# Kernel tuning notes

Hardware: AMD Instinct MI355X
Metric: run time of the kernel (lower is better)

Reference implementation:

```python
import jax, jax.numpy as jnp
import numpy as np

SPLINE_ORDER = 3


def _bspline_basis(x, knots, k, order):
    """Cox-de Boor recursion with static (python float) knots, matching the torch code exactly."""
    if order == 0:
        if k + 1 >= len(knots):
            return jnp.zeros_like(x)
        return ((knots[k] <= x) & (x < knots[k + 1])).astype(x.dtype)
    left = 0.0
    right = 0.0
    if k + order < len(knots) and knots[k + order] != knots[k]:
        left = (x - knots[k]) / (knots[k + order] - knots[k]) * _bspline_basis(x, knots, k, order - 1)
    if k + order + 1 < len(knots) and knots[k + order + 1] != knots[k + 1]:
        right = (knots[k + order + 1] - x) / (knots[k + order + 1] - knots[k + 1]) * _bspline_basis(x, knots, k + 1, order - 1)
    return left + right


def setup_inputs() -> dict:
    key = jax.random.key(0)
    k1, k2, k3 = jax.random.split(key, 3)
    B, S, IN, OUT, NUM_KNOTS = 16, 4096, 256, 256, 5
    x = jax.random.normal(k1, (B, S, IN), dtype=jnp.float32)
    inner_coeffs = jax.random.normal(k2, (IN, NUM_KNOTS), dtype=jnp.float32) * 0.1
    outer_coeffs = jax.random.normal(k3, (OUT, IN), dtype=jnp.float32) * 0.1
    return {"x": x, "inner_coeffs": inner_coeffs, "outer_coeffs": outer_coeffs}


def reference(x, inner_coeffs, outer_coeffs):
    in_dim, num_knots = inner_coeffs.shape
    # knots = linspace(-1, 1, num_knots + spline_order), static python floats
    knots = np.linspace(-1.0, 1.0, num_knots + SPLINE_ORDER).tolist()
    xt = jnp.tanh(x)  # [B, S, I]
    # Original loops k in range(num_knots - spline_order); remaining basis columns stay zero,
    # so only the first n_active inner coefficients contribute.
    n_active = num_knots - SPLINE_ORDER
    basis = jnp.stack(
        [_bspline_basis(xt, knots, k, SPLINE_ORDER) for k in range(n_active)], axis=-1
    )  # [B, S, I, n_active]
    inner = jnp.einsum('bsik,ik->bsi', basis, inner_coeffs[:, :n_active])  # [B, S, I]
    return jnp.einsum('bsi,oi->bso', inner, outer_coeffs)  # [B, S, O]
```

## Files before the change

kernel.cpp:

```cpp
#include <hip/hip_runtime.h>
#include <hip/hip_bf16.h>
#include <stdint.h>


typedef __attribute__((ext_vector_type(8))) short short8;
typedef __attribute__((ext_vector_type(4))) float f32x4;

__device__ __forceinline__ uint16_t f2bf(float f) {
    union { float f; uint32_t u; } v; v.f = f;
    uint32_t r = v.u + 0x7FFFu + ((v.u >> 16) & 1u);
    return (uint16_t)(r >> 16);
}

__device__ __forceinline__ uint32_t pack_bf2(float lo, float hi) {
    __hip_bfloat162 h = __float22bfloat162_rn(make_float2(lo, hi));
    union { __hip_bfloat162 h; uint32_t u; } v; v.h = h;
    return v.u;
}

__device__ __forceinline__ float cube_relu(float v) {
    float m = fmaxf(v, 0.0f);
    return m * m * m;
}

__device__ __forceinline__ float inner_eval(float xx, float c0, float c1) {
    float e  = __expf(2.0f * xx);
    float t  = 1.0f - 2.0f * __builtin_amdgcn_rcpf(e + 1.0f);
    float u  = (t + 1.0f) * 3.5f;
    float w0 = cube_relu(u);
    float w1 = cube_relu(u - 1.0f);
    float w2 = cube_relu(u - 2.0f);
    float w3 = cube_relu(u - 3.0f);
    float w4 = cube_relu(u - 4.0f);
    float w5 = cube_relu(u - 5.0f);
    float B0 = w0 - 4.0f*w1 + 6.0f*w2 - 4.0f*w3 + w4;
    float B1 = w1 - 4.0f*w2 + 6.0f*w3 - 4.0f*w4 + w5;
    return (c0 * B0 + c1 * B1) * (1.0f / 6.0f);
}

__device__ __forceinline__ void load_lds16(const void* g, void* l) {
    __builtin_amdgcn_global_load_lds(
        (const __attribute__((address_space(1))) uint32_t*)g,
        (__attribute__((address_space(3))) uint32_t*)l, 16, 0, 0);
}

__global__ void conv_w(const float4* __restrict__ wf, char* __restrict__ o) {
    const int i = blockIdx.x * blockDim.x + threadIdx.x;
    const float4 v = wf[i];
    uint2 r;
    r.x = (uint32_t)f2bf(v.x) | ((uint32_t)f2bf(v.y) << 16);
    r.y = (uint32_t)f2bf(v.z) | ((uint32_t)f2bf(v.w) << 16);
    const int row = i >> 6;
    const int cb  = (i & 63) << 3;
    *(uint2*)(o + row * 512 + (cb ^ ((row & 7) << 4))) = r;
}

__global__ void __launch_bounds__(512, 2) kan_fused(const float* __restrict__ x,
                                                    const float* __restrict__ ic,
                                                    const char* __restrict__ wb,
                                                    float* __restrict__ out)
{
    __shared__ __align__(16) char Wlds[131072];
    __shared__ __align__(16) float2 C2[256];

    const int t    = threadIdx.x;
    const int lane = t & 63;
    const int w    = t >> 6;
    const int mrow = lane & 15;
    const int quad = lane >> 4;

    if (t < 256) C2[t] = make_float2(ic[t * 5 + 0], ic[t * 5 + 1]);

    const float* xp0 = x + (size_t)(blockIdx.x * 256 + w * 16 + mrow) * 256 + quad * 8;
    float4 xa = *(const float4*)(xp0);
    float4 xb = *(const float4*)(xp0 + 4);

    #pragma unroll
    for (int it = 0; it < 16; ++it) {
        const int base = ((it * 8 + w) << 10) + lane * 16;
        load_lds16(wb + base, Wlds + base);
    }
    __syncthreads();

    const int cbase = quad * 16;
    const int swz   = (mrow & 7) << 4;

    #pragma unroll 1
    for (int s = 0; s < 2; ++s) {
        const int mbase = blockIdx.x * 256 + (s * 8 + w) * 16;
        const float* xp = x + (size_t)(mbase + mrow) * 256 + quad * 8;
        if (s) {
            xa = *(const float4*)(xp);
            xb = *(const float4*)(xp + 4);
        }

        f32x4 acc[16];
        #pragma unroll
        for (int j = 0; j < 16; ++j) acc[j] = (f32x4){0.f, 0.f, 0.f, 0.f};

        #pragma unroll 1
        for (int kk = 0; kk < 8; ++kk) {
            const int cw = (kk * 64 + cbase) ^ swz;
            short8 b[16];
            #pragma unroll
            for (int j = 0; j < 16; ++j)
                b[j] = *(const short8*)(Wlds + (j * 16 + mrow) * 512 + cw);

            float4 xa_n = xa, xb_n = xb;
            if (kk < 7) {
                xa_n = *(const float4*)(xp + kk * 32 + 32);
                xb_n = *(const float4*)(xp + kk * 32 + 36);
            }

            const int gk = kk * 32 + quad * 8;
            const float4 cA = *(const float4*)(&C2[gk + 0]);
            const float4 cB = *(const float4*)(&C2[gk + 2]);
            const float4 cC = *(const float4*)(&C2[gk + 4]);
            const float4 cD = *(const float4*)(&C2[gk + 6]);

            float v0 = inner_eval(xa.x, cA.x, cA.y);
            float v1 = inner_eval(xa.y, cA.z, cA.w);
            float v2 = inner_eval(xa.z, cB.x, cB.y);
            float v3 = inner_eval(xa.w, cB.z, cB.w);
            float v4 = inner_eval(xb.x, cC.x, cC.y);
            float v5 = inner_eval(xb.y, cC.z, cC.w);
            float v6 = inner_eval(xb.z, cD.x, cD.y);
            float v7 = inner_eval(xb.w, cD.z, cD.w);

            union { short8 v; uint32_t u[4]; } af;
            af.u[0] = pack_bf2(v0, v1);
            af.u[1] = pack_bf2(v2, v3);
            af.u[2] = pack_bf2(v4, v5);
            af.u[3] = pack_bf2(v6, v7);

            #pragma unroll
            for (int j = 0; j < 16; ++j)
                acc[j] = __builtin_amdgcn_mfma_f32_16x16x32_bf16(af.v, b[j], acc[j], 0, 0, 0);

            xa = xa_n; xb = xb_n;
        }

        float* op = out + (size_t)(mbase + quad * 4) * 256 + mrow;
        #pragma unroll
        for (int j = 0; j < 16; ++j) {
            #pragma unroll
            for (int r = 0; r < 4; ++r)
                op[(size_t)r * 256 + j * 16] = acc[j][r];
        }
    }
}

extern "C" void kernel_launch(void* const* d_in, const int* in_sizes, int n_in,
                              void* d_out, int out_size, void* d_ws, size_t ws_size,
                              hipStream_t stream) {
    const float* x  = (const float*)d_in[0];
    const float* ic = (const float*)d_in[1];
    const float* oc = (const float*)d_in[2];
    char* wb = (char*)d_ws;

    conv_w<<<64, 256, 0, stream>>>((const float4*)oc, wb);
    kan_fused<<<256, 512, 0, stream>>>(x, ic, wb, (float*)d_out);
}
```

Measured before the change: 130.8 us.

## Hoist spline evaluation ahead of MFMA loop and prefetch second tile inputs

```diff
diff --git a/kernel.cpp b/kernel.cpp
--- a/kernel.cpp
+++ b/kernel.cpp
@@ -44,7 +44,8 @@
         (__attribute__((address_space(3))) uint32_t*)l, 16, 0, 0);
 }
 
-__global__ void conv_w(const float4* __restrict__ wf, char* __restrict__ o) {
+__global__ void conv_w(const float* __restrict__ ic, const float4* __restrict__ wf,
+                       char* __restrict__ o) {
     const int i = blockIdx.x * blockDim.x + threadIdx.x;
     const float4 v = wf[i];
     uint2 r;
@@ -53,101 +54,126 @@
     const int row = i >> 6;
     const int cb  = (i & 63) << 3;
     *(uint2*)(o + row * 512 + (cb ^ ((row & 7) << 4))) = r;
+    if (i < 256)
+        *(float2*)(o + 131072 + i * 8) = make_float2(ic[i * 5 + 0], ic[i * 5 + 1]);
+}
+
+__device__ __forceinline__ short8 spline8(float4 xa, float4 xb, const float2* C2, int gk) {
+    const float4 cA = *(const float4*)(&C2[gk + 0]);
+    const float4 cB = *(const float4*)(&C2[gk + 2]);
+    const float4 cC = *(const float4*)(&C2[gk + 4]);
+    const float4 cD = *(const float4*)(&C2[gk + 6]);
+    float v0 = inner_eval(xa.x, cA.x, cA.y);
+    float v1 = inner_eval(xa.y, cA.z, cA.w);
+    float v2 = inner_eval(xa.z, cB.x, cB.y);
+    float v3 = inner_eval(xa.w, cB.z, cB.w);
+    float v4 = inner_eval(xb.x, cC.x, cC.y);
+    float v5 = inner_eval(xb.y, cC.z, cC.w);
+    float v6 = inner_eval(xb.z, cD.x, cD.y);
+    float v7 = inner_eval(xb.w, cD.z, cD.w);
+    union { short8 v; uint32_t u[4]; } af;
+    af.u[0] = pack_bf2(v0, v1);
+    af.u[1] = pack_bf2(v2, v3);
+    af.u[2] = pack_bf2(v4, v5);
+    af.u[3] = pack_bf2(v6, v7);
+    return af.v;
+}
+
+__device__ __forceinline__ void mfma_store(const short8* af, const char* Wlds,
+                                           float* __restrict__ out, int mbase,
+                                           int mrow, int quad, int swz) {
+    f32x4 acc[16];
+    #pragma unroll
+    for (int j = 0; j < 16; ++j) acc[j] = (f32x4){0.f, 0.f, 0.f, 0.f};
+
+    #pragma unroll
+    for (int kk = 0; kk < 8; ++kk) {
+        const int cw = (kk * 64 + quad * 16) ^ swz;
+        short8 bg[8];
+        #pragma unroll
+        for (int j = 0; j < 8; ++j)
+            bg[j] = *(const short8*)(Wlds + ((j * 16 + mrow) << 9) + cw);
+        #pragma unroll
+        for (int j = 0; j < 8; ++j)
+            acc[j] = __builtin_amdgcn_mfma_f32_16x16x32_bf16(af[kk], bg[j], acc[j], 0, 0, 0);
+        #pragma unroll
+        for (int j = 0; j < 8; ++j)
+            bg[j] = *(const short8*)(Wlds + (((j + 8) * 16 + mrow) << 9) + cw);
+        #pragma unroll
+        for (int j = 0; j < 8; ++j)
+            acc[j + 8] = __builtin_amdgcn_mfma_f32_16x16x32_bf16(af[kk], bg[j], acc[j + 8], 0, 0, 0);
+    }
+
+    float* op = out + (size_t)(mbase + quad * 4) * 256 + mrow;
+    #pragma unroll
+    for (int j = 0; j < 16; ++j) {
+        #pragma unroll
+        for (int r = 0; r < 4; ++r)
+            op[(size_t)r * 256 + j * 16] = acc[j][r];
+    }
 }
 
 __global__ void __launch_bounds__(512, 2) kan_fused(const float* __restrict__ x,
-                                                    const float* __restrict__ ic,
                                                     const char* __restrict__ wb,
                                                     float* __restrict__ out)
 {
-    __shared__ __align__(16) char Wlds[131072];
-    __shared__ __align__(16) float2 C2[256];
+    __shared__ __align__(16) char smem[133120];
+    char*   Wlds = smem;
+    float2* C2   = (float2*)(smem + 131072);
 
     const int t    = threadIdx.x;
     const int lane = t & 63;
     const int w    = t >> 6;
     const int mrow = lane & 15;
     const int quad = lane >> 4;
+    const int swz  = (mrow & 7) << 4;
 
-    if (t < 256) C2[t] = make_float2(ic[t * 5 + 0], ic[t * 5 + 1]);
+    const int mb0 = blockIdx.x * 256 + w * 16;
+    const int mb1 = mb0 + 128;
 
-    const float* xp0 = x + (size_t)(blockIdx.x * 256 + w * 16 + mrow) * 256 + quad * 8;
-    float4 xa = *(const float4*)(xp0);
-    float4 xb = *(const float4*)(xp0 + 4);
+    const float* xr0 = x + (size_t)(mb0 + mrow) * 256 + quad * 8;
+    const float* xr1 = x + (size_t)(mb1 + mrow) * 256 + quad * 8;
+
+    float4 xv[16];
+    #pragma unroll
+    for (int kk = 0; kk < 8; ++kk) {
+        xv[2 * kk]     = *(const float4*)(xr0 + kk * 32);
+        xv[2 * kk + 1] = *(const float4*)(xr0 + kk * 32 + 4);
+    }
+
+    const float4* c2g = (const float4*)(wb + 131072);
+    const float4 cg0 = c2g[lane * 2];
+    const float4 cg1 = c2g[lane * 2 + 1];
 
     #pragma unroll
     for (int it = 0; it < 16; ++it) {
         const int base = ((it * 8 + w) << 10) + lane * 16;
         load_lds16(wb + base, Wlds + base);
     }
+
+    *(float4*)((char*)C2 + lane * 32)      = cg0;
+    *(float4*)((char*)C2 + lane * 32 + 16) = cg1;
+
+    short8 af[8];
+    #pragma unroll
+    for (int kk = 0; kk < 8; ++kk)
+        af[kk] = spline8(xv[2 * kk], xv[2 * kk + 1], C2, kk * 32 + quad * 8);
+
     __syncthreads();
 
-    const int cbase = quad * 16;
-    const int swz   = (mrow & 7) << 4;
+    #pragma unroll
+    for (int kk = 0; kk < 8; ++kk) {
+        xv[2 * kk]     = *(const float4*)(xr1 + kk * 32);
+        xv[2 * kk + 1] = *(const float4*)(xr1 + kk * 32 + 4);
+    }
 
-    #pragma unroll 1
-    for (int s = 0; s < 2; ++s) {
-        const int mbase = blockIdx.x * 256 + (s * 8 + w) * 16;
-        const float* xp = x + (size_t)(mbase + mrow) * 256 + quad * 8;
-        if (s) {
-            xa = *(const float4*)(xp);
-            xb = *(const float4*)(xp + 4);
-        }
+    mfma_store(af, Wlds, out, mb0, mrow, quad, swz);
 
-        f32x4 acc[16];
-        #pragma unroll
-        for (int j = 0; j < 16; ++j) acc[j] = (f32x4){0.f, 0.f, 0.f, 0.f};
+    #pragma unroll
+    for (int kk = 0; kk < 8; ++kk)
+        af[kk] = spline8(xv[2 * kk], xv[2 * kk + 1], C2, kk * 32 + quad * 8);
 
-        #pragma unroll 1
-        for (int kk = 0; kk < 8; ++kk) {
-            const int cw = (kk * 64 + cbase) ^ swz;
-            short8 b[16];
-            #pragma unroll
-            for (int j = 0; j < 16; ++j)
-                b[j] = *(const short8*)(Wlds + (j * 16 + mrow) * 512 + cw);
-
-            float4 xa_n = xa, xb_n = xb;
-            if (kk < 7) {
-                xa_n = *(const float4*)(xp + kk * 32 + 32);
-                xb_n = *(const float4*)(xp + kk * 32 + 36);
-            }
-
-            const int gk = kk * 32 + quad * 8;
-            const float4 cA = *(const float4*)(&C2[gk + 0]);
-            const float4 cB = *(const float4*)(&C2[gk + 2]);
-            const float4 cC = *(const float4*)(&C2[gk + 4]);
-            const float4 cD = *(const float4*)(&C2[gk + 6]);
-
-            float v0 = inner_eval(xa.x, cA.x, cA.y);
-            float v1 = inner_eval(xa.y, cA.z, cA.w);
-            float v2 = inner_eval(xa.z, cB.x, cB.y);
-            float v3 = inner_eval(xa.w, cB.z, cB.w);
-            float v4 = inner_eval(xb.x, cC.x, cC.y);
-            float v5 = inner_eval(xb.y, cC.z, cC.w);
-            float v6 = inner_eval(xb.z, cD.x, cD.y);
-            float v7 = inner_eval(xb.w, cD.z, cD.w);
-
-            union { short8 v; uint32_t u[4]; } af;
-            af.u[0] = pack_bf2(v0, v1);
-            af.u[1] = pack_bf2(v2, v3);
-            af.u[2] = pack_bf2(v4, v5);
-            af.u[3] = pack_bf2(v6, v7);
-
-            #pragma unroll
-            for (int j = 0; j < 16; ++j)
-                acc[j] = __builtin_amdgcn_mfma_f32_16x16x32_bf16(af.v, b[j], acc[j], 0, 0, 0);
-
-            xa = xa_n; xb = xb_n;
-        }
-
-        float* op = out + (size_t)(mbase + quad * 4) * 256 + mrow;
-        #pragma unroll
-        for (int j = 0; j < 16; ++j) {
-            #pragma unroll
-            for (int r = 0; r < 4; ++r)
-                op[(size_t)r * 256 + j * 16] = acc[j][r];
-        }
-    }
+    mfma_store(af, Wlds, out, mb1, mrow, quad, swz);
 }
 
 extern "C" void kernel_launch(void* const* d_in, const int* in_sizes, int n_in,
@@ -158,6 +184,6 @@
     const float* oc = (const float*)d_in[2];
     char* wb = (char*)d_ws;
 
-    conv_w<<<64, 256, 0, stream>>>((const float4*)oc, wb);
-    kan_fused<<<256, 512, 0, stream>>>(x, ic, wb, (float*)d_out);
+    conv_w<<<64, 256, 0, stream>>>(ic, (const float4*)oc, wb);
+    kan_fused<<<256, 512, 0, stream>>>(x, wb, (float*)d_out);
 }
```

New measurement: 208.6 us. 59.5% more time.
